# Performance work log

Hardware: AMD Instinct MI355X
Metric: run time of the kernel (lower is better)

Reference implementation:

```python
import jax, jax.numpy as jnp
import numpy as np

B, N, C = 4, 2048, 1024
H = 16
D = C // H  # head dim = 64

def setup_inputs() -> dict:
    key = jax.random.key(0)
    k1, k2, k3 = jax.random.split(key, 3)
    x = jax.random.normal(k1, (B, N, C), dtype=jnp.float32)
    w_attn = jax.random.normal(k2, (C, 3 * C), dtype=jnp.float32) * (C ** -0.5)
    w_proj = jax.random.normal(k3, (C, C), dtype=jnp.float32) * (C ** -0.5)
    return {"x": x, "w_attn": w_attn, "w_proj": w_proj}

def reference(x, w_attn, w_proj):
    # fused QKV projection (bias=False)
    qkv = jnp.einsum('bnc,cf->bnf', x, w_attn)            # [B,N,3C]
    q, k, v = jnp.split(qkv, 3, axis=-1)                  # each [B,N,C]
    # [B,H,N,D]
    q = q.reshape(B, N, H, D).transpose(0, 2, 1, 3)
    k = k.reshape(B, N, H, D).transpose(0, 2, 1, 3)
    v = v.reshape(B, N, H, D).transpose(0, 2, 1, 3)
    # scaled dot-product attention, non-causal, no mask, dropout_p=0
    scale = 1.0 / jnp.sqrt(jnp.asarray(D, dtype=q.dtype))
    scores = jnp.einsum('bhqd,bhkd->bhqk', q, k) * scale  # [B,H,N,N]
    attn = jax.nn.softmax(scores, axis=-1)
    y = jnp.einsum('bhqk,bhkd->bhqd', attn, v)            # [B,H,N,D]
    y = y.transpose(0, 2, 1, 3).reshape(B, N, C)
    # output projection (bias=False); resid dropout is identity at p=0
    return jnp.einsum('bnc,co->bno', y, w_proj)
```

## Files before the change

kernel.cpp:

```cpp
#include <hip/hip_runtime.h>
#include <hip/hip_bf16.h>

typedef __hip_bfloat16 bf16;
typedef short short8 __attribute__((ext_vector_type(8)));
typedef float f32x4 __attribute__((ext_vector_type(4)));

#define GLOBAL_AS __attribute__((address_space(1)))
#define LDS_AS __attribute__((address_space(3)))

__device__ inline unsigned short f2bf(float x) {
    union { float f; unsigned u; } v; v.f = x;
    unsigned r = v.u + 0x7fffu + ((v.u >> 16) & 1u);
    return (unsigned short)(r >> 16);
}

__device__ inline unsigned pkbf(float a, float b) {
    float2 f; f.x = a; f.y = b;
    union { __hip_bfloat162 h; unsigned u; } c;
    c.h = __float22bfloat162_rn(f);
    return c.u;
}

__device__ inline float fast_exp2(float x) {
#if __has_builtin(__builtin_amdgcn_exp2f)
    return __builtin_amdgcn_exp2f(x);
#else
    return exp2f(x);
#endif
}

__device__ inline void async16(const void* g, void* l) {
    __builtin_amdgcn_global_load_lds((const GLOBAL_AS void*)g, (LDS_AS void*)l, 16, 0, 0);
}


__global__ __launch_bounds__(256) void cvt_f32_bf16(const float* __restrict__ in,
                                                    unsigned short* __restrict__ out, int n4) {
    int i = blockIdx.x * 256 + threadIdx.x;
    if (i < n4) {
        float4 v = ((const float4*)in)[i];
        ushort4 o;
        o.x = f2bf(v.x); o.y = f2bf(v.y); o.z = f2bf(v.z); o.w = f2bf(v.w);
        ((ushort4*)out)[i] = o;
    }
}

__global__ __launch_bounds__(256) void transpose_bf16(const float* __restrict__ in,
                                                      unsigned short* __restrict__ out,
                                                      int R, int Cc) {
    __shared__ float s[32][33];
    int tx = threadIdx.x & 31, ty = threadIdx.x >> 5;
    int c0 = blockIdx.x * 32, r0 = blockIdx.y * 32;
#pragma unroll
    for (int i = 0; i < 4; i++)
        s[ty + i * 8][tx] = in[(size_t)(r0 + ty + i * 8) * Cc + c0 + tx];
    __syncthreads();
#pragma unroll
    for (int i = 0; i < 4; i++)
        out[(size_t)(c0 + ty + i * 8) * R + r0 + tx] = f2bf(s[tx][ty + i * 8]);
}


template <int MODE>
__global__ __launch_bounds__(256) void gemm_bf16(const bf16* __restrict__ A,
                                                 const bf16* __restrict__ Bt,
                                                 unsigned short* __restrict__ outQ,
                                                 unsigned short* __restrict__ outK,
                                                 unsigned short* __restrict__ outV,
                                                 float* __restrict__ outF, float qscale) {
    const int KD = 1024;
    __shared__ __align__(16) char smem[34816];
    bf16* sA = (bf16*)smem;
    bf16* sB = (bf16*)(smem + 16384);
    const int t = threadIdx.x;
    const int w = t >> 6, lane = t & 63, l15 = lane & 15, qd = lane >> 4;
    const int bn = blockIdx.x, bm = blockIdx.y;
    const int wm = (w >> 1) * 64, wn = (w & 1) * 64;
    const int sw = l15 & 7;

    f32x4 acc[4][4];
#pragma unroll
    for (int i = 0; i < 4; i++)
#pragma unroll
        for (int j = 0; j < 4; j++) acc[i][j] = (f32x4){0.f, 0.f, 0.f, 0.f};

    const int rsub = lane >> 3;
    const int csrc = ((lane & 7) ^ rsub) << 3;
    const bf16* Ab = A + (size_t)(bm * 128 + w * 32 + rsub) * KD + csrc;
    const bf16* Bb = Bt + (size_t)(bn * 128 + w * 32 + rsub) * KD + csrc;
    bf16* sAw = sA + (w * 32) * 64;
    bf16* sBw = sB + (w * 32) * 64;

    for (int kt = 0; kt < 16; ++kt) {
#pragma unroll
        for (int j = 0; j < 4; ++j) {
            async16(Ab + (size_t)(j * 8) * KD + kt * 64, sAw + j * 512);
            async16(Bb + (size_t)(j * 8) * KD + kt * 64, sBw + j * 512);
        }
        __syncthreads();
#pragma unroll
        for (int ks = 0; ks < 2; ++ks) {
            const int cphys = (((ks * 4 + qd) ^ sw) << 3);
            short8 af[4], bfv[4];
#pragma unroll
            for (int mi = 0; mi < 4; mi++)
                af[mi] = *(const short8*)&sA[(wm + mi * 16 + l15) * 64 + cphys];
#pragma unroll
            for (int ni = 0; ni < 4; ni++)
                bfv[ni] = *(const short8*)&sB[(wn + ni * 16 + l15) * 64 + cphys];
#pragma unroll
            for (int mi = 0; mi < 4; mi++)
#pragma unroll
                for (int ni = 0; ni < 4; ni++)
                    acc[mi][ni] = __builtin_amdgcn_mfma_f32_16x16x32_bf16(af[mi], bfv[ni],
                                                                          acc[mi][ni], 0, 0, 0);
        }
        __syncthreads();
    }

    if (MODE == 0) {
        unsigned short* sC = (unsigned short*)smem;
        const int part = bn >> 3;
        const int hb = (bn & 7) * 2;
        if (part < 2) {
            const float sc = (part == 0) ? qscale : 1.0f;
            unsigned short* dst = (part == 0) ? outQ : outK;
#pragma unroll
            for (int mi = 0; mi < 4; mi++)
#pragma unroll
                for (int ni = 0; ni < 4; ni++)
#pragma unroll
                    for (int r = 0; r < 4; r++)
                        sC[(wm + mi * 16 + qd * 4 + r) * 136 + wn + ni * 16 + l15] =
                            f2bf(acc[mi][ni][r] * sc);
            __syncthreads();
#pragma unroll
            for (int i = 0; i < 8; i++) {
                const int j = t + i * 256;
                const int row = j >> 4, c16 = j & 15;
                uint4 v = *(const uint4*)&sC[row * 136 + c16 * 8];
                const int m = bm * 128 + row;
                const int b = m >> 11, ns = m & 2047;
                const int h = hb + (c16 >> 3);
                const int dd = (c16 & 7) * 8;
                *(uint4*)&dst[((size_t)(b * 16 + h) * 2048 + ns) * 64 + dd] = v;
            }
        } else {
#pragma unroll
            for (int ni = 0; ni < 4; ni++)
#pragma unroll
                for (int mi = 0; mi < 4; mi++) {
                    uint2 pk;
                    pk.x = (unsigned)f2bf(acc[mi][ni][0]) | ((unsigned)f2bf(acc[mi][ni][1]) << 16);
                    pk.y = (unsigned)f2bf(acc[mi][ni][2]) | ((unsigned)f2bf(acc[mi][ni][3]) << 16);
                    *(uint2*)&sC[(wn + ni * 16 + l15) * 136 + wm + mi * 16 + qd * 4] = pk;
                }
            __syncthreads();
            const int m0b = bm * 128;
            const int b = m0b >> 11, ns0 = m0b & 2047;
#pragma unroll
            for (int i = 0; i < 8; i++) {
                const int j = t + i * 256;
                const int f = j >> 4, tc = j & 15;
                uint4 v = *(const uint4*)&sC[f * 136 + tc * 8];
                const int h = hb + (f >> 6), dd = f & 63;
                *(uint4*)&outV[((size_t)(b * 16 + h) * 64 + dd) * 2048 + ns0 + tc * 8] = v;
            }
        }
    } else {
        float* sF = (float*)smem;
#pragma unroll
        for (int pass = 0; pass < 2; ++pass) {
            if (pass) __syncthreads();
            if ((wm >> 6) == pass) {
#pragma unroll
                for (int mi = 0; mi < 4; mi++)
#pragma unroll
                    for (int ni = 0; ni < 4; ni++)
#pragma unroll
                        for (int r = 0; r < 4; r++)
                            sF[(mi * 16 + qd * 4 + r) * 132 + wn + ni * 16 + l15] =
                                acc[mi][ni][r];
            }
            __syncthreads();
#pragma unroll
            for (int i = 0; i < 8; i++) {
                const int j = t + i * 256;
                const int row = j >> 5, c4 = j & 31;
                float4 v = *(const float4*)&sF[row * 132 + c4 * 4];
                *(float4*)&outF[(size_t)(bm * 128 + pass * 64 + row) * 1024 + bn * 128 +
                                c4 * 4] = v;
            }
        }
    }
}


__global__ __launch_bounds__(256) void attn_kernel(const bf16* __restrict__ Q,
                                                   const bf16* __restrict__ K,
                                                   const bf16* __restrict__ Vt,
                                                   bf16* __restrict__ Y) {
    const int blk = blockIdx.x;
    const int bh = (blk & 7) * 8 + (blk >> 7);
    const int qt = (blk >> 3) & 15;
    const int b = bh >> 4, h = bh & 15;
    const int t = threadIdx.x, w = t >> 6, lane = t & 63, l15 = lane & 15, qd = lane >> 4;
    const int swz = l15 & 7;

    __shared__ __align__(16) char smem[51200];
    bf16* sK = (bf16*)smem;
    bf16* sVt = (bf16*)(smem + 16384);
    bf16* sP = (bf16*)(smem + 32768) + w * 2304;
    bf16* sO = (bf16*)(smem + 32768);

    const size_t bhbase = (size_t)bh * 2048 * 64;

    short8 qf[2][2];
#pragma unroll
    for (int mi = 0; mi < 2; mi++)
#pragma unroll
        for (int ks = 0; ks < 2; ks++)
            qf[mi][ks] = *(const short8*)(Q + bhbase +
                                          (size_t)(qt * 128 + w * 32 + mi * 16 + l15) * 64 +
                                          ks * 32 + qd * 8);

    f32x4 ot[4][2];
#pragma unroll
    for (int i = 0; i < 4; i++)
#pragma unroll
        for (int j = 0; j < 2; j++) ot[i][j] = (f32x4){0.f, 0.f, 0.f, 0.f};
    float l_run[2] = {0.f, 0.f};

    const int rsub = lane >> 3;
    const bf16* Kb = K + bhbase + (size_t)(w * 32 + rsub) * 64 + (((lane & 7) ^ rsub) << 3);
    bf16* sKw = sK + (w * 32) * 64;
    const int dsub = lane >> 4, cch = lane & 15;
    const bf16* Vb = Vt + (size_t)bh * 64 * 2048;

    for (int kt = 0; kt < 16; ++kt) {
#pragma unroll
        for (int j = 0; j < 4; ++j)
            async16(Kb + (size_t)kt * 8192 + j * 512, sKw + j * 512);
#pragma unroll
        for (int j = 0; j < 4; ++j) {
            const int d = w * 16 + j * 4 + dsub;
            async16(Vb + (size_t)d * 2048 + kt * 128 + ((cch ^ (d & 7)) << 3),
                    sVt + (w * 16 + j * 4) * 128);
        }
        __syncthreads();

#pragma unroll
        for (int half = 0; half < 2; ++half) {
            f32x4 accS[4][2];
#pragma unroll
            for (int i = 0; i < 4; i++)
#pragma unroll
                for (int j = 0; j < 2; j++) accS[i][j] = (f32x4){0.f, 0.f, 0.f, 0.f};
#pragma unroll
            for (int ks = 0; ks < 2; ks++) {
                const int cph = (((ks * 4 + qd) ^ swz) << 3);
#pragma unroll
                for (int kt2 = 0; kt2 < 4; kt2++) {
                    short8 kf =
                        *(const short8*)&sK[((half * 4 + kt2) * 16 + l15) * 64 + cph];
                    accS[kt2][0] = __builtin_amdgcn_mfma_f32_16x16x32_bf16(kf, qf[0][ks],
                                                                           accS[kt2][0], 0, 0, 0);
                    accS[kt2][1] = __builtin_amdgcn_mfma_f32_16x16x32_bf16(kf, qf[1][ks],
                                                                           accS[kt2][1], 0, 0, 0);
                }
            }
#pragma unroll
            for (int mi = 0; mi < 2; mi++) {
                float ls = 0.f;
#pragma unroll
                for (int kt2 = 0; kt2 < 4; kt2++) {
                    float p0 = fast_exp2(accS[kt2][mi][0]);
                    float p1 = fast_exp2(accS[kt2][mi][1]);
                    float p2 = fast_exp2(accS[kt2][mi][2]);
                    float p3 = fast_exp2(accS[kt2][mi][3]);
                    ls += (p0 + p1) + (p2 + p3);
                    uint2 pk;
                    pk.x = pkbf(p0, p1);
                    pk.y = pkbf(p2, p3);
                    *(uint2*)&sP[(mi * 16 + l15) * 72 + kt2 * 16 + qd * 4] = pk;
                }
                l_run[mi] += ls;
            }
#pragma unroll
            for (int kk = 0; kk < 2; kk++) {
                short8 pf0 = *(const short8*)&sP[l15 * 72 + kk * 32 + qd * 8];
                short8 pf1 = *(const short8*)&sP[(16 + l15) * 72 + kk * 32 + qd * 8];
#pragma unroll
                for (int mi2 = 0; mi2 < 4; mi2++) {
                    short8 vf = *(const short8*)&sVt[(mi2 * 16 + l15) * 128 +
                                                     (((half * 8 + kk * 4 + qd) ^ swz) << 3)];
                    ot[mi2][0] =
                        __builtin_amdgcn_mfma_f32_16x16x32_bf16(vf, pf0, ot[mi2][0], 0, 0, 0);
                    ot[mi2][1] =
                        __builtin_amdgcn_mfma_f32_16x16x32_bf16(vf, pf1, ot[mi2][1], 0, 0, 0);
                }
            }
        }
        __syncthreads();
    }

    float rl[2];
#pragma unroll
    for (int mi = 0; mi < 2; mi++) {
        float l = l_run[mi];
        l += __shfl_xor(l, 16);
        l += __shfl_xor(l, 32);
        rl[mi] = 1.f / l;
    }
#pragma unroll
    for (int ni2 = 0; ni2 < 2; ni2++) {
#pragma unroll
        for (int mi2 = 0; mi2 < 4; mi2++) {
            uint2 pk;
            pk.x = pkbf(ot[mi2][ni2][0] * rl[ni2], ot[mi2][ni2][1] * rl[ni2]);
            pk.y = pkbf(ot[mi2][ni2][2] * rl[ni2], ot[mi2][ni2][3] * rl[ni2]);
            *(uint2*)&sO[(w * 32 + ni2 * 16 + l15) * 72 + mi2 * 16 + qd * 4] = pk;
        }
    }
    __syncthreads();
#pragma unroll
    for (int i = 0; i < 4; i++) {
        int row = (t >> 3) + i * 32, doff = (t & 7) * 8;
        uint4 vv = *(const uint4*)&sO[row * 72 + doff];
        *(uint4*)(Y + ((size_t)(b * 2048 + qt * 128 + row)) * 1024 + h * 64 + doff) = vv;
    }
}


extern "C" void kernel_launch(void* const* d_in, const int* in_sizes, int n_in,
                              void* d_out, int out_size, void* d_ws, size_t ws_size,
                              hipStream_t stream) {
    const float* x = (const float*)d_in[0];
    const float* w_attn = (const float*)d_in[1];
    const float* w_proj = (const float*)d_in[2];
    float* out = (float*)d_out;
    char* ws = (char*)d_ws;

    bf16* xb = (bf16*)(ws);
    bf16* waT = (bf16*)(ws + 16777216);
    bf16* wpT = (bf16*)(ws + 23068672);
    bf16* qb = (bf16*)(ws + 25165824);
    bf16* kb = (bf16*)(ws + 41943040);
    bf16* vtb = (bf16*)(ws + 58720256);

    cvt_f32_bf16<<<8192, 256, 0, stream>>>(x, (unsigned short*)xb, 2097152);
    transpose_bf16<<<dim3(96, 32), 256, 0, stream>>>(w_attn, (unsigned short*)waT, 1024, 3072);
    transpose_bf16<<<dim3(32, 32), 256, 0, stream>>>(w_proj, (unsigned short*)wpT, 1024, 1024);

    const float qscale = 0.125f * 1.44269504088896340736f;
    gemm_bf16<0><<<dim3(24, 64), 256, 0, stream>>>(xb, waT, (unsigned short*)qb,
                                                   (unsigned short*)kb, (unsigned short*)vtb,
                                                   nullptr, qscale);
    attn_kernel<<<dim3(1024), 256, 0, stream>>>(qb, kb, vtb, xb );
    gemm_bf16<1><<<dim3(8, 64), 256, 0, stream>>>(xb, wpT, nullptr, nullptr, nullptr, out, 1.0f);
}
```

Measured before the change: 292.6 us.

## Switch attention to 32x32x16 MFMA and keep P in registers via lane shuffles

Rewrites the attention inner loop to use 32x32x16 bf16 MFMA tiles instead of 16x16x32. The softmax probabilities are now redistributed between half-waves with shuffles rather than staged through an LDS buffer, which drops the per-wave sP scratch and cuts shared memory from 50KB to 32KB. This removes LDS round-trips for P and may allow higher occupancy. It relies on the compiler handling the larger accumulators well, and register pressure could rise.

Measured after the change: 287.7 us. About the same (-1.7%).

```diff
diff --git a/kernel.cpp b/kernel.cpp
--- a/kernel.cpp
+++ b/kernel.cpp
@@ -4,6 +4,7 @@
 typedef __hip_bfloat16 bf16;
 typedef short short8 __attribute__((ext_vector_type(8)));
 typedef float f32x4 __attribute__((ext_vector_type(4)));
+typedef float f32x16 __attribute__((ext_vector_type(16)));
 
 #define GLOBAL_AS __attribute__((address_space(1)))
 #define LDS_AS __attribute__((address_space(3)))
@@ -203,39 +204,35 @@
     const int blk = blockIdx.x;
     const int bh = (blk & 7) * 8 + (blk >> 7);
     const int qt = (blk >> 3) & 15;
-    const int b = bh >> 4, h = bh & 15;
-    const int t = threadIdx.x, w = t >> 6, lane = t & 63, l15 = lane & 15, qd = lane >> 4;
-    const int swz = l15 & 7;
-
-    __shared__ __align__(16) char smem[51200];
+    const int b = bh >> 4, h16 = bh & 15;
+    const int t = threadIdx.x, w = t >> 6, lane = t & 63;
+    const int c = lane & 31, hl = lane >> 5;
+    const int sw = c & 7;
+    const bool hi = hl != 0;
+
+    __shared__ __align__(16) char smem[32768];
     bf16* sK = (bf16*)smem;
     bf16* sVt = (bf16*)(smem + 16384);
-    bf16* sP = (bf16*)(smem + 32768) + w * 2304;
-    bf16* sO = (bf16*)(smem + 32768);
+    bf16* sO = (bf16*)smem;
 
     const size_t bhbase = (size_t)bh * 2048 * 64;
 
-    short8 qf[2][2];
-#pragma unroll
-    for (int mi = 0; mi < 2; mi++)
-#pragma unroll
-        for (int ks = 0; ks < 2; ks++)
-            qf[mi][ks] = *(const short8*)(Q + bhbase +
-                                          (size_t)(qt * 128 + w * 32 + mi * 16 + l15) * 64 +
-                                          ks * 32 + qd * 8);
-
-    f32x4 ot[4][2];
-#pragma unroll
-    for (int i = 0; i < 4; i++)
-#pragma unroll
-        for (int j = 0; j < 2; j++) ot[i][j] = (f32x4){0.f, 0.f, 0.f, 0.f};
-    float l_run[2] = {0.f, 0.f};
+    short8 qf[4];
+#pragma unroll
+    for (int kc = 0; kc < 4; kc++)
+        qf[kc] = *(const short8*)(Q + bhbase + (size_t)(qt * 128 + w * 32 + c) * 64 +
+                                  kc * 16 + hl * 8);
+
+    f32x16 ot[2];
+#pragma unroll
+    for (int i = 0; i < 16; i++) { ot[0][i] = 0.f; ot[1][i] = 0.f; }
+    float l_run = 0.f;
 
     const int rsub = lane >> 3;
     const bf16* Kb = K + bhbase + (size_t)(w * 32 + rsub) * 64 + (((lane & 7) ^ rsub) << 3);
     bf16* sKw = sK + (w * 32) * 64;
     const int dsub = lane >> 4, cch = lane & 15;
-    const bf16* Vb = Vt + (size_t)bh * 64 * 2048;
+    const bf16* Vb = Vt + bhbase;
 
     for (int kt = 0; kt < 16; ++kt) {
 #pragma unroll
@@ -250,84 +247,69 @@
         __syncthreads();
 
 #pragma unroll
-        for (int half = 0; half < 2; ++half) {
-            f32x4 accS[4][2];
-#pragma unroll
-            for (int i = 0; i < 4; i++)
-#pragma unroll
-                for (int j = 0; j < 2; j++) accS[i][j] = (f32x4){0.f, 0.f, 0.f, 0.f};
-#pragma unroll
-            for (int ks = 0; ks < 2; ks++) {
-                const int cph = (((ks * 4 + qd) ^ swz) << 3);
-#pragma unroll
-                for (int kt2 = 0; kt2 < 4; kt2++) {
-                    short8 kf =
-                        *(const short8*)&sK[((half * 4 + kt2) * 16 + l15) * 64 + cph];
-                    accS[kt2][0] = __builtin_amdgcn_mfma_f32_16x16x32_bf16(kf, qf[0][ks],
-                                                                           accS[kt2][0], 0, 0, 0);
-                    accS[kt2][1] = __builtin_amdgcn_mfma_f32_16x16x32_bf16(kf, qf[1][ks],
-                                                                           accS[kt2][1], 0, 0, 0);
-                }
-            }
-#pragma unroll
-            for (int mi = 0; mi < 2; mi++) {
-                float ls = 0.f;
-#pragma unroll
-                for (int kt2 = 0; kt2 < 4; kt2++) {
-                    float p0 = fast_exp2(accS[kt2][mi][0]);
-                    float p1 = fast_exp2(accS[kt2][mi][1]);
-                    float p2 = fast_exp2(accS[kt2][mi][2]);
-                    float p3 = fast_exp2(accS[kt2][mi][3]);
-                    ls += (p0 + p1) + (p2 + p3);
-                    uint2 pk;
-                    pk.x = pkbf(p0, p1);
-                    pk.y = pkbf(p2, p3);
-                    *(uint2*)&sP[(mi * 16 + l15) * 72 + kt2 * 16 + qd * 4] = pk;
-                }
-                l_run[mi] += ls;
-            }
-#pragma unroll
-            for (int kk = 0; kk < 2; kk++) {
-                short8 pf0 = *(const short8*)&sP[l15 * 72 + kk * 32 + qd * 8];
-                short8 pf1 = *(const short8*)&sP[(16 + l15) * 72 + kk * 32 + qd * 8];
-#pragma unroll
-                for (int mi2 = 0; mi2 < 4; mi2++) {
-                    short8 vf = *(const short8*)&sVt[(mi2 * 16 + l15) * 128 +
-                                                     (((half * 8 + kk * 4 + qd) ^ swz) << 3)];
-                    ot[mi2][0] =
-                        __builtin_amdgcn_mfma_f32_16x16x32_bf16(vf, pf0, ot[mi2][0], 0, 0, 0);
-                    ot[mi2][1] =
-                        __builtin_amdgcn_mfma_f32_16x16x32_bf16(vf, pf1, ot[mi2][1], 0, 0, 0);
-                }
+        for (int kt2 = 0; kt2 < 4; ++kt2) {
+            f32x16 accS;
+#pragma unroll
+            for (int i = 0; i < 16; i++) accS[i] = 0.f;
+#pragma unroll
+            for (int kc = 0; kc < 4; kc++) {
+                short8 kf =
+                    *(const short8*)&sK[(kt2 * 32 + c) * 64 + (((kc * 2 + hl) ^ sw) << 3)];
+                accS = __builtin_amdgcn_mfma_f32_32x32x16_bf16(kf, qf[kc], accS, 0, 0, 0);
+            }
+            float p[16];
+            float ls = 0.f;
+#pragma unroll
+            for (int i = 0; i < 16; i++) {
+                p[i] = fast_exp2(accS[i]);
+                ls += p[i];
+            }
+            l_run += ls;
+            unsigned u[8], e[8];
+#pragma unroll
+            for (int i = 0; i < 8; i++) u[i] = pkbf(p[2 * i], p[2 * i + 1]);
+#pragma unroll
+            for (int i = 0; i < 8; i++) e[i] = (unsigned)__shfl_xor((int)u[i], 32, 64);
+            union { uint4 u4; short8 s8; } F0, F1;
+            F0.u4.x = hi ? e[2] : u[0];
+            F0.u4.y = hi ? e[3] : u[1];
+            F0.u4.z = hi ? u[2] : e[0];
+            F0.u4.w = hi ? u[3] : e[1];
+            F1.u4.x = hi ? e[6] : u[4];
+            F1.u4.y = hi ? e[7] : u[5];
+            F1.u4.z = hi ? u[6] : e[4];
+            F1.u4.w = hi ? u[7] : e[5];
+#pragma unroll
+            for (int mi2 = 0; mi2 < 2; mi2++) {
+                short8 vf0 = *(const short8*)&sVt[(mi2 * 32 + c) * 128 +
+                                                  (((kt2 * 4 + hl) ^ sw) << 3)];
+                ot[mi2] = __builtin_amdgcn_mfma_f32_32x32x16_bf16(vf0, F0.s8, ot[mi2], 0, 0, 0);
+                short8 vf1 = *(const short8*)&sVt[(mi2 * 32 + c) * 128 +
+                                                  (((kt2 * 4 + 2 + hl) ^ sw) << 3)];
+                ot[mi2] = __builtin_amdgcn_mfma_f32_32x32x16_bf16(vf1, F1.s8, ot[mi2], 0, 0, 0);
             }
         }
         __syncthreads();
     }
 
-    float rl[2];
-#pragma unroll
-    for (int mi = 0; mi < 2; mi++) {
-        float l = l_run[mi];
-        l += __shfl_xor(l, 16);
-        l += __shfl_xor(l, 32);
-        rl[mi] = 1.f / l;
-    }
-#pragma unroll
-    for (int ni2 = 0; ni2 < 2; ni2++) {
-#pragma unroll
-        for (int mi2 = 0; mi2 < 4; mi2++) {
+    float l = l_run + __shfl_xor(l_run, 32, 64);
+    float rl = 1.f / l;
+#pragma unroll
+    for (int mi2 = 0; mi2 < 2; mi2++)
+#pragma unroll
+        for (int q4 = 0; q4 < 4; q4++) {
+            const int d0 = mi2 * 32 + q4 * 8 + hl * 4;
             uint2 pk;
-            pk.x = pkbf(ot[mi2][ni2][0] * rl[ni2], ot[mi2][ni2][1] * rl[ni2]);
-            pk.y = pkbf(ot[mi2][ni2][2] * rl[ni2], ot[mi2][ni2][3] * rl[ni2]);
-            *(uint2*)&sO[(w * 32 + ni2 * 16 + l15) * 72 + mi2 * 16 + qd * 4] = pk;
-        }
-    }
+            pk.x = pkbf(ot[mi2][q4 * 4 + 0] * rl, ot[mi2][q4 * 4 + 1] * rl);
+            pk.y = pkbf(ot[mi2][q4 * 4 + 2] * rl, ot[mi2][q4 * 4 + 3] * rl);
+            *(uint2*)&sO[(w * 32 + c) * 72 + d0] = pk;
+        }
     __syncthreads();
 #pragma unroll
     for (int i = 0; i < 4; i++) {
         int row = (t >> 3) + i * 32, doff = (t & 7) * 8;
         uint4 vv = *(const uint4*)&sO[row * 72 + doff];
-        *(uint4*)(Y + ((size_t)(b * 2048 + qt * 128 + row)) * 1024 + h * 64 + doff) = vv;
+        *(uint4*)(Y + ((size_t)(b * 2048 + qt * 128 + row)) * 1024 + h16 * 64 + doff) = vv;
     }
 }
 
```
